# Optimization experiments

Measured on AMD Instinct MI355X. Metric: run time of the kernel, lower is better.

The kernel has to match this reference:

```python
import jax, jax.numpy as jnp
import numpy as np

N = 50000
E = 800000
CIN = 32
COUT = 64
DIM = 2
KS = 5                      # kernel size per pseudo-coordinate dim
K = KS ** DIM               # 25 kernel weight matrices
DEGREE = 1
S = (DEGREE + 1) ** DIM     # 4 nonzero B-spline basis products per edge


def _spline_basis(pseudo):
    # pseudo: [E, DIM] in [0, 1]; open linear (degree-1) B-splines per dim.
    v = pseudo * (KS - DEGREE)                              # [E, DIM]
    lo = jnp.floor(v)
    frac = v - lo                                           # [E, DIM]
    lo = jnp.clip(lo.astype(jnp.int32), 0, KS - 2)          # guard p == 1
    bits = (jnp.arange(S)[:, None] >> jnp.arange(DIM)[None, :]) & 1   # [S, DIM]
    # tensor-product basis values: [E, S]
    b = jnp.where(bits[None].astype(bool), frac[:, None, :], 1.0 - frac[:, None, :])
    basis = jnp.prod(b, axis=-1)
    offsets = (KS ** jnp.arange(DIM)).astype(jnp.int32)     # flat-index strides
    wi = jnp.sum((lo[:, None, :] + bits[None]) * offsets[None, None, :], axis=-1)  # [E, S]
    return basis, wi


def setup_inputs() -> dict:
    key = jax.random.key(0)
    k1, k2, k3, k4, k5, k6 = jax.random.split(key, 6)
    bound = 1.0 / np.sqrt(CIN * K)
    x = jax.random.normal(k1, (N, CIN), dtype=jnp.float32)
    edge_index = jax.random.randint(k2, (2, E), 0, N, dtype=jnp.int64)
    pseudo = jax.random.uniform(k3, (E, DIM), dtype=jnp.float32)
    weight = jax.random.uniform(k4, (K, CIN, COUT), minval=-bound, maxval=bound, dtype=jnp.float32)
    root = jax.random.uniform(k5, (CIN, COUT), minval=-bound, maxval=bound, dtype=jnp.float32)
    bias = jax.random.uniform(k6, (COUT,), minval=-bound, maxval=bound, dtype=jnp.float32)
    return {"x": x, "edge_index": edge_index, "pseudo": pseudo,
            "weight": weight, "root": root, "bias": bias}


def reference(x, edge_index, pseudo, weight, root, bias):
    n, cin = x.shape
    cout = weight.shape[-1]
    row = edge_index[0]   # destination nodes (scatter target)
    col = edge_index[1]   # source nodes (gather)
    basis, wi = _spline_basis(pseudo)                       # [E, S], [E, S]
    # Transform every node by every kernel weight matrix: [N, K, Cout]
    y = jnp.einsum('ni,kio->nko', x, weight)
    flat = y.reshape(n * K, cout)
    g = flat[col[:, None] * K + wi]                         # [E, S, Cout] gather
    msg = jnp.einsum('es,eso->eo', basis, g)                # [E, Cout]
    out = jax.ops.segment_sum(msg, row, num_segments=n)     # scatter-add to dst
    deg = jax.ops.segment_sum(jnp.ones((row.shape[0],), dtype=x.dtype), row, num_segments=n)
    out = out / jnp.maximum(deg, 1.0)[:, None]              # degree normalization
    out = out + x @ root + bias                             # root transform + bias
    return out
```

## Files before the change

kernel.cpp:

```cpp
#include <hip/hip_runtime.h>

#define N_NODES 50000
#define E_EDGES 800000
#define CIN     32
#define COUT    64
#define NB      16
#define BCAP    54016
#define NCB     196
#define RCAP    4864
#define KPAD    136
#define SCANB   1024
#define NSCANBLK ((N_NODES + SCANB - 1) / SCANB)
#define EPB     8
#define BBLK    ((E_EDGES + EPB * 256 - 1) / (EPB * 256))
#define XCHUNK  (N_NODES * CIN / 4)

typedef __attribute__((ext_vector_type(8))) short s8v;
typedef __attribute__((ext_vector_type(4))) float f4v;
typedef __attribute__((ext_vector_type(4))) unsigned short u4v;

static __device__ inline unsigned short f2bf(float f) {
    unsigned u = __builtin_bit_cast(unsigned, f);
    u += 0x7fff + ((u >> 16) & 1);
    return (unsigned short)(u >> 16);
}
static __device__ inline float bf2f(unsigned short h) {
    unsigned u = ((unsigned)h) << 16;
    return __builtin_bit_cast(float, u);
}
static __device__ inline unsigned f2bf2(float a, float b) {
    return (unsigned)f2bf(a) | ((unsigned)f2bf(b) << 16);
}


__global__ __launch_bounds__(256) void build_recs(
    const float* __restrict__ x, unsigned short* __restrict__ xbf,
    const int* __restrict__ ei, const float* __restrict__ pseudo,
    int* __restrict__ cursor, int* __restrict__ cursR,
    unsigned long long* __restrict__ recs, unsigned* __restrict__ rp)
{
    {
        const int cb = blockIdx.x * 1024;
#pragma unroll
        for (int k = 0; k < 4; ++k) {
            const int i = cb + k * 256 + threadIdx.x;
            if (i < XCHUNK) {
                f4v v = *(const f4v*)(x + (size_t)i * 4);
                union { unsigned u2[2]; u4v v4; } o;
                o.u2[0] = f2bf2(v[0], v[1]);
                o.u2[1] = f2bf2(v[2], v[3]);
                *(u4v*)(xbf + (size_t)i * 4) = o.v4;
            }
        }
    }

    __shared__ int lh[NB];
    __shared__ int lbase[NB];
    __shared__ int lh2[NCB];
    __shared__ int lbase2[NCB];
    if (threadIdx.x < NB) lh[threadIdx.x] = 0;
    if (threadIdx.x < NCB) lh2[threadIdx.x] = 0;
    __syncthreads();

    const int ebase0 = blockIdx.x * (EPB * 256);
    unsigned long long rcache[EPB];
    int pcache[EPB];
    int pcache2[EPB];

#pragma unroll
    for (int i = 0; i < EPB; ++i) {
        const int e = ebase0 + i * 256 + threadIdx.x;
        pcache[i] = -1; pcache2[i] = -1;
        if (e < E_EDGES) {
            const int row = min(max(ei[e], 0), N_NODES - 1);
            const int col = min(max(ei[E_EDGES + e], 0), N_NODES - 1);
            const float v0 = pseudo[2 * e] * 4.0f, v1 = pseudo[2 * e + 1] * 4.0f;
            const float fl0 = floorf(v0), fl1 = floorf(v1);
            const int lo0 = min(max((int)fl0, 0), 3);
            const int lo1 = min(max((int)fl1, 0), 3);
            const int f0q = min((int)((v0 - fl0) * 65536.0f), 65535);
            const int f1q = min((int)((v1 - fl1) * 65536.0f), 65535);
            const int b = lo0 + 4 * lo1;
            rcache[i] = (unsigned long long)row
                      | ((unsigned long long)col << 16)
                      | ((unsigned long long)f0q << 32)
                      | ((unsigned long long)f1q << 48);
            pcache[i]  = b | (atomicAdd(&lh[b], 1) << 8);
            const int cb = row >> 8;
            pcache2[i] = cb | (atomicAdd(&lh2[cb], 1) << 8);
        }
    }
    __syncthreads();

    if (threadIdx.x < NB)
        lbase[threadIdx.x] = atomicAdd(&cursor[threadIdx.x], lh[threadIdx.x]);
    if (threadIdx.x < NCB)
        lbase2[threadIdx.x] = atomicAdd(&cursR[threadIdx.x], lh2[threadIdx.x]);
    __syncthreads();

#pragma unroll
    for (int i = 0; i < EPB; ++i) {
        if (pcache[i] >= 0) {
            const int b = pcache[i] & 0xFF;
            const int idx = min(lbase[b] + (pcache[i] >> 8), BCAP - 1);
            const unsigned recslot = (unsigned)(b * BCAP + idx);
            recs[recslot] = rcache[i];
            const int cb = pcache2[i] & 0xFF;
            const int idx2 = min(lbase2[cb] + (pcache2[i] >> 8), RCAP - 1);
            const unsigned rowlow = (unsigned)(rcache[i] & 0xFF);
            rp[(size_t)cb * RCAP + idx2] = recslot | (rowlow << 20);
        }
    }
}

__global__ __launch_bounds__(256) void deg_hist(
    const unsigned* __restrict__ rp, const int* __restrict__ cursR,
    int* __restrict__ degi)
{
    __shared__ int h[256];
    h[threadIdx.x] = 0;
    __syncthreads();
    const int cb = blockIdx.x;
    const int cnt = min(cursR[cb], RCAP);
    const unsigned* bp = rp + (size_t)cb * RCAP;
    for (int i = threadIdx.x; i < cnt; i += 256)
        atomicAdd(&h[bp[i] >> 20], 1);
    __syncthreads();
    const int row = cb * 256 + threadIdx.x;
    if (row < N_NODES) degi[row] = h[threadIdx.x];
}

__global__ __launch_bounds__(1024) void scan_blocks(
    const int* __restrict__ degi, int* __restrict__ rowstart, int* __restrict__ bsum)
{
    __shared__ int wsum[16];
    __shared__ int woff[16];
    const int tid = threadIdx.x, lane = tid & 63, wid = tid >> 6;
    const int n = blockIdx.x * SCANB + tid;
    const int v = (n < N_NODES) ? degi[n] : 0;
    int val = v;
#pragma unroll
    for (int off = 1; off < 64; off <<= 1) {
        int t = __shfl_up(val, off);
        if (lane >= off) val += t;
    }
    if (lane == 63) wsum[wid] = val;
    __syncthreads();
    if (tid == 0) {
        int a = 0;
#pragma unroll
        for (int w = 0; w < 16; ++w) { woff[w] = a; a += wsum[w]; }
        bsum[blockIdx.x] = a;
    }
    __syncthreads();
    if (n < N_NODES) rowstart[n] = woff[wid] + (val - v);
}

__global__ __launch_bounds__(1024) void scan_finish(
    int* __restrict__ rowstart, const int* __restrict__ bsum)
{
    const int b = blockIdx.x;
    int off = 0;
    for (int i = 0; i < NSCANBLK; ++i)
        off += (i < b) ? bsum[i] : 0;
    const int n = b * SCANB + threadIdx.x;
    if (n < N_NODES) rowstart[n] += off;
    if (b == NSCANBLK - 1 && threadIdx.x == 0)
        rowstart[N_NODES] = off + bsum[NSCANBLK - 1];
}

__global__ __launch_bounds__(256) void rank_write(
    const unsigned* __restrict__ rp, const int* __restrict__ cursR,
    const int* __restrict__ rowstart, unsigned* __restrict__ eidx)
{
    __shared__ int cur[256];
    const int cb = blockIdx.x;
    const int row = cb * 256 + threadIdx.x;
    cur[threadIdx.x] = (row < N_NODES) ? rowstart[row] : 0;
    __syncthreads();
    const int cnt = min(cursR[cb], RCAP);
    const unsigned* bp = rp + (size_t)cb * RCAP;
    for (int i = threadIdx.x; i < cnt; i += 256) {
        const unsigned e = bp[i];
        const int pos = min(atomicAdd(&cur[e >> 20], 1), E_EDGES - 1);
        eidx[pos] = e & 0xFFFFF;
    }
}

__global__ __launch_bounds__(256, 2) void bucket_mfma_seq(
    const unsigned short* __restrict__ xbf, const float* __restrict__ weight,
    const unsigned long long* __restrict__ recs,
    const int* __restrict__ cursor, const int* __restrict__ degi,
    unsigned short* __restrict__ msg)
{
    __shared__ short XS[4][16 * KPAD];

    const int lane = threadIdx.x & 63;
    const int wid  = threadIdx.x >> 6;
    const int cell = blockIdx.x & (NB - 1);
    const int wGlob   = (blockIdx.x >> 4) * 4 + wid;
    const int wStride = (gridDim.x >> 4) * 4;
    const int eg = lane >> 2, part = lane & 3;

    const int lo0 = cell & 3, lo1 = cell >> 2;
    const int base = lo0 + 5 * lo1;
    const int offs[4] = {0, 1, 5, 6};
    const int q = lane >> 4;
    const int c = lane & 15;

    s8v bfr[4][4];
#pragma unroll
    for (int s = 0; s < 4; ++s) {
        const float* wp = weight + (size_t)(base + offs[s]) * (CIN * COUT);
#pragma unroll
        for (int nt = 0; nt < 4; ++nt) {
            union { unsigned short u[8]; s8v v; } tmp;
#pragma unroll
            for (int j = 0; j < 8; ++j)
                tmp.u[j] = f2bf(wp[(q * 8 + j) * COUT + nt * 16 + c]);
            bfr[s][nt] = tmp.v;
        }
    }

    const unsigned long long* brec = recs + (size_t)cell * BCAP;
    const int cnt    = min(cursor[cell], BCAP);
    const int ntiles = (cnt + 15) >> 4;

    int t = wGlob;
    unsigned long long rec_c = 0;
    int deg_c = 1;
    s8v x_c = {};
    if (t < ntiles) {
        rec_c = brec[min(t * 16 + eg, cnt - 1)];
        deg_c = degi[(int)(rec_c & 0xFFFF)];
        x_c = *(const s8v*)(xbf + (size_t)((rec_c >> 16) & 0xFFFF) * CIN + part * 8);
    }

    for (; t < ntiles; t += wStride) {
        const int tn = t + wStride;
        unsigned long long rec_n = 0;
        int deg_n = 1;
        if (tn < ntiles) {
            rec_n = brec[min(tn * 16 + eg, cnt - 1)];
            deg_n = degi[(int)(rec_n & 0xFFFF)];
        }

        const bool vcur = (t * 16 + eg) < cnt;
        const float f0 = (float)(int)((rec_c >> 32) & 0xFFFF) * (1.0f / 65536.0f);
        const float f1 = (float)(int)((rec_c >> 48) & 0xFFFF) * (1.0f / 65536.0f);
        const float invd = vcur ? (1.0f / (float)max(deg_c, 1)) : 0.0f;
        const float s0 = (1.0f - f0) * (1.0f - f1) * invd;
        const float s1 = f0 * (1.0f - f1) * invd;
        const float s2 = (1.0f - f0) * f1 * invd;
        const float s3 = f0 * f1 * invd;

        {
            union { unsigned short u[8]; s8v v; } xin; xin.v = x_c;
            float xv[8];
#pragma unroll
            for (int j = 0; j < 8; ++j) xv[j] = bf2f(xin.u[j]);
            short* dst = &XS[wid][eg * KPAD + part * 8];
            const float ss[4] = {s0, s1, s2, s3};
#pragma unroll
            for (int s = 0; s < 4; ++s) {
                union { unsigned u2[4]; s8v v; } tmp;
#pragma unroll
                for (int j = 0; j < 8; j += 2)
                    tmp.u2[j >> 1] = f2bf2(ss[s] * xv[j], ss[s] * xv[j + 1]);
                *(s8v*)(dst + s * 32) = tmp.v;
            }
        }
        __builtin_amdgcn_wave_barrier();

        s8v afr[4];
        {
            const short* ap = &XS[wid][c * KPAD + q * 8];
#pragma unroll
            for (int ks = 0; ks < 4; ++ks)
                afr[ks] = *(const s8v*)(ap + ks * 32);
        }
        __builtin_amdgcn_wave_barrier();

        s8v x_n = {};
        if (tn < ntiles)
            x_n = *(const s8v*)(xbf + (size_t)((rec_n >> 16) & 0xFFFF) * CIN + part * 8);

        f4v acc[4];
#pragma unroll
        for (int nt = 0; nt < 4; ++nt) {
            acc[nt] = (f4v){0.f, 0.f, 0.f, 0.f};
#pragma unroll
            for (int ks = 0; ks < 4; ++ks)
                acc[nt] = __builtin_amdgcn_mfma_f32_16x16x32_bf16(
                    afr[ks], bfr[ks][nt], acc[nt], 0, 0, 0);
        }

#pragma unroll
        for (int r = 0; r < 4; ++r) {
            const int m = q * 4 + r;
#pragma unroll
            for (int nt = 0; nt < 4; ++nt)
                XS[wid][m * 64 + nt * 16 + c] = (short)f2bf(acc[nt][r]);
        }
        __builtin_amdgcn_wave_barrier();
        {
            const short* sp = &XS[wid][eg * 64 + part * 16];
            s8v vlo = *(const s8v*)sp;
            s8v vhi = *(const s8v*)(sp + 8);
            unsigned short* dst = msg
                + ((size_t)cell * BCAP + (size_t)t * 16 + eg) * COUT + part * 16;
            *(s8v*)dst = vlo;
            *(s8v*)(dst + 8) = vhi;
        }
        __builtin_amdgcn_wave_barrier();

        rec_c = rec_n; deg_c = deg_n; x_c = x_n;
    }
}

__global__ __launch_bounds__(256) void gather_perm(
    const unsigned short* __restrict__ msg, const unsigned* __restrict__ eidx,
    const int* __restrict__ rowstart, const float* __restrict__ x,
    const float* __restrict__ root, const float* __restrict__ bias,
    float* __restrict__ out)
{
    const int wave   = (blockIdx.x * blockDim.x + threadIdx.x) >> 6;
    const int lane   = threadIdx.x & 63;
    const int nwaves = (gridDim.x * blockDim.x) >> 6;

    for (int n = wave; n < N_NODES; n += nwaves) {
        const int s  = rowstart[n];
        const int e2 = rowstart[n + 1];
        float acc = 0.f;
#pragma unroll 8
        for (int p = s; p < e2; ++p) {
            const unsigned slot = eidx[p];
            acc += bf2f(msg[(size_t)slot * COUT + lane]);
        }
        const float* xp = x + (size_t)n * CIN;
        float rt = bias[lane];
#pragma unroll
        for (int i = 0; i < CIN; ++i)
            rt += xp[i] * root[i * COUT + lane];
        out[(size_t)n * COUT + lane] = acc + rt;
    }
}


__global__ __launch_bounds__(256) void count_fb(
    const int* __restrict__ ei, const float* __restrict__ pseudo,
    int* __restrict__ hist, float* __restrict__ deg)
{
    __shared__ int lh[16];
    if (threadIdx.x < 16) lh[threadIdx.x] = 0;
    __syncthreads();
    const int e = blockIdx.x * 256 + threadIdx.x;
    if (e < E_EDGES) {
        int row = min(max(ei[e], 0), N_NODES - 1);
        const float v0 = pseudo[2 * e] * 4.0f, v1 = pseudo[2 * e + 1] * 4.0f;
        const int lo0 = min(max((int)floorf(v0), 0), 3);
        const int lo1 = min(max((int)floorf(v1), 0), 3);
        atomicAdd(&lh[lo0 + 4 * lo1], 1);
        atomicAdd(&deg[row], 1.0f);
    }
    __syncthreads();
    if (threadIdx.x < 16) atomicAdd(&hist[threadIdx.x], lh[threadIdx.x]);
}

__global__ void scan16_fb(const int* __restrict__ hist,
                          int* __restrict__ bstart, int* __restrict__ cursor)
{
    if (threadIdx.x == 0 && blockIdx.x == 0) {
        int acc = 0;
        for (int c = 0; c < 16; ++c) { bstart[c] = acc; cursor[c] = acc; acc += hist[c]; }
    }
}

__global__ __launch_bounds__(256) void scatter_fb(
    const float* __restrict__ pseudo, int* __restrict__ cursor, int* __restrict__ list)
{
    __shared__ int lh[16];
    __shared__ int lbase[16];
    if (threadIdx.x < 16) lh[threadIdx.x] = 0;
    __syncthreads();
    const int e = blockIdx.x * 256 + threadIdx.x;
    int cell = 0, myoff = 0;
    if (e < E_EDGES) {
        const float v0 = pseudo[2 * e] * 4.0f, v1 = pseudo[2 * e + 1] * 4.0f;
        const int lo0 = min(max((int)floorf(v0), 0), 3);
        const int lo1 = min(max((int)floorf(v1), 0), 3);
        cell = lo0 + 4 * lo1;
        myoff = atomicAdd(&lh[cell], 1);
    }
    __syncthreads();
    if (threadIdx.x < 16)
        lbase[threadIdx.x] = atomicAdd(&cursor[threadIdx.x], lh[threadIdx.x]);
    __syncthreads();
    if (e < E_EDGES)
        list[lbase[cell] + myoff] = e;
}

__global__ __launch_bounds__(256, 2) void bucket_mfma_fb(
    const float* __restrict__ x, const int* __restrict__ ei,
    const float* __restrict__ pseudo, const float* __restrict__ weight,
    const int* __restrict__ list, const int* __restrict__ bstart,
    const int* __restrict__ hist, float* __restrict__ out)
{
    __shared__ short XS[4][16 * KPAD];
    const int lane = threadIdx.x & 63;
    const int wid  = threadIdx.x >> 6;
    const int beta = blockIdx.x & 15;
    const int wGlob   = (blockIdx.x >> 4) * 4 + wid;
    const int wStride = (gridDim.x >> 4) * 4;
    const int lo0 = beta & 3, lo1 = beta >> 2;
    const int base = lo0 + 5 * lo1;
    const int offs[4] = {0, 1, 5, 6};
    const int q = lane >> 4, c = lane & 15;

    s8v bfr[4][4];
#pragma unroll
    for (int s = 0; s < 4; ++s) {
        const float* wp = weight + (size_t)(base + offs[s]) * (CIN * COUT);
#pragma unroll
        for (int nt = 0; nt < 4; ++nt) {
            union { unsigned short u[8]; s8v v; } tmp;
#pragma unroll
            for (int j = 0; j < 8; ++j)
                tmp.u[j] = f2bf(wp[(q * 8 + j) * COUT + nt * 16 + c]);
            bfr[s][nt] = tmp.v;
        }
    }
    const int start = bstart[beta], cnt = hist[beta];
    const int ntiles = (cnt + 15) >> 4;

    for (int t = wGlob; t < ntiles; t += wStride) {
        const int ebase = start + t * 16;
        int rowv = 0, colv = 0;
        float b0 = 0.f, b1 = 0.f, b2 = 0.f, b3 = 0.f;
        if (lane < 16 && (t * 16 + lane) < cnt) {
            const int e = list[ebase + lane];
            rowv = min(max(ei[e], 0), N_NODES - 1);
            colv = min(max(ei[E_EDGES + e], 0), N_NODES - 1);
            const float v0 = pseudo[2 * e] * 4.0f, v1 = pseudo[2 * e + 1] * 4.0f;
            const float f0 = v0 - floorf(v0), f1 = v1 - floorf(v1);
            b0 = (1.0f - f0) * (1.0f - f1);
            b1 = f0 * (1.0f - f1);
            b2 = (1.0f - f0) * f1;
            b3 = f0 * f1;
        }
        {
            const int eg = lane >> 2, part = lane & 3;
            const int  gc = __shfl(colv, eg);
            const float ss0 = __shfl(b0, eg), ss1 = __shfl(b1, eg);
            const float ss2 = __shfl(b2, eg), ss3 = __shfl(b3, eg);
            const float ss[4] = {ss0, ss1, ss2, ss3};
            const float* xp = x + (size_t)gc * CIN + part * 8;
            float xv[8];
            *(f4v*)&xv[0] = *(const f4v*)xp;
            *(f4v*)&xv[4] = *(const f4v*)(xp + 4);
            short* dst = &XS[wid][eg * KPAD + part * 8];
#pragma unroll
            for (int s = 0; s < 4; ++s) {
                union { unsigned short u[8]; s8v v; } tmp;
#pragma unroll
                for (int j = 0; j < 8; ++j)
                    tmp.u[j] = f2bf(ss[s] * xv[j]);
                *(s8v*)(dst + s * 32) = tmp.v;
            }
        }
        __builtin_amdgcn_wave_barrier();
        s8v afr[4];
        {
            const short* ap = &XS[wid][c * KPAD + q * 8];
#pragma unroll
            for (int ks = 0; ks < 4; ++ks)
                afr[ks] = *(const s8v*)(ap + ks * 32);
        }
        __builtin_amdgcn_wave_barrier();
        f4v acc[4];
#pragma unroll
        for (int nt = 0; nt < 4; ++nt) {
            acc[nt] = (f4v){0.f, 0.f, 0.f, 0.f};
#pragma unroll
            for (int ks = 0; ks < 4; ++ks)
                acc[nt] = __builtin_amdgcn_mfma_f32_16x16x32_bf16(
                    afr[ks], bfr[ks][nt], acc[nt], 0, 0, 0);
        }
#pragma unroll
        for (int r = 0; r < 4; ++r) {
            const int m = q * 4 + r;
            const int orow = __shfl(rowv, m);
#pragma unroll
            for (int nt = 0; nt < 4; ++nt)
                atomicAdd(&out[(size_t)orow * COUT + nt * 16 + c], acc[nt][r]);
        }
    }
}

__global__ __launch_bounds__(256) void final_fb(
    const float* __restrict__ x, const float* __restrict__ root,
    const float* __restrict__ bias, const float* __restrict__ deg,
    float* __restrict__ out)
{
    const int wave   = (blockIdx.x * blockDim.x + threadIdx.x) >> 6;
    const int lane   = threadIdx.x & 63;
    const int nwaves = (gridDim.x * blockDim.x) >> 6;
    for (int n = wave; n < N_NODES; n += nwaves) {
        const float* xp = x + (size_t)n * CIN;
        float acc = bias[lane];
#pragma unroll
        for (int i = 0; i < CIN; ++i)
            acc += xp[i] * root[i * COUT + lane];
        float dg = deg[n];
        dg = dg > 1.0f ? dg : 1.0f;
        const size_t idx = (size_t)n * COUT + lane;
        out[idx] = out[idx] / dg + acc;
    }
}

extern "C" void kernel_launch(void* const* d_in, const int* in_sizes, int n_in,
                              void* d_out, int out_size, void* d_ws, size_t ws_size,
                              hipStream_t stream) {
    const float* x      = (const float*)d_in[0];
    const int*   ei     = (const int*)d_in[1];
    const float* pseudo = (const float*)d_in[2];
    const float* weight = (const float*)d_in[3];
    const float* root   = (const float*)d_in[4];
    const float* bias   = (const float*)d_in[5];
    float* out = (float*)d_out;

    int* wsI = (int*)d_ws;
    int* cursor16 = wsI;
    int* cursR    = wsI + 32;
    int* degi     = wsI + 256;
    int* rowstart = wsI + 50256;
    int* bsum     = wsI + 100272;
    unsigned long long* recs = (unsigned long long*)((char*)d_ws + 401408);
    unsigned* rp   = (unsigned*)((char*)d_ws + 401408 + (size_t)NB * BCAP * 8);
    unsigned* eidx = (unsigned*)((char*)rp + (size_t)NCB * RCAP * 4);
    unsigned short* xbf = (unsigned short*)((char*)eidx + (size_t)E_EDGES * 4);
    unsigned short* msg = (unsigned short*)((char*)xbf + (size_t)N_NODES * CIN * 2);
    const size_t needed = 401408 + (size_t)NB * BCAP * 8 + (size_t)NCB * RCAP * 4
                        + (size_t)E_EDGES * 4 + (size_t)N_NODES * CIN * 2
                        + (size_t)NB * BCAP * COUT * 2;

    if (ws_size >= needed) {
        (void)hipMemsetAsync(d_ws, 0, 256 * 4, stream);
        build_recs <<<BBLK, 256, 0, stream>>>(x, xbf, ei, pseudo, cursor16, cursR, recs, rp);
        deg_hist   <<<NCB, 256, 0, stream>>>(rp, cursR, degi);
        scan_blocks<<<NSCANBLK, 1024, 0, stream>>>(degi, rowstart, bsum);
        scan_finish<<<NSCANBLK, 1024, 0, stream>>>(rowstart, bsum);
        rank_write <<<NCB, 256, 0, stream>>>(rp, cursR, rowstart, eidx);
        bucket_mfma_seq<<<16 * 128, 256, 0, stream>>>(
            xbf, weight, recs, cursor16, degi, msg);
        gather_perm<<<4096, 256, 0, stream>>>(msg, eidx, rowstart, x, root, bias, out);
    } else {
        char* w = (char*)d_ws;
        float* degF   = (float*)w;
        int*   histF  = (int*)(w + 200064);
        int*   bstF   = (int*)(w + 200128);
        int*   curF   = (int*)(w + 200192);
        int*   listF  = (int*)(w + 200256);
        const int eblocks = (E_EDGES + 255) / 256;

        (void)hipMemsetAsync(out, 0, sizeof(float) * (size_t)N_NODES * COUT, stream);
        (void)hipMemsetAsync(degF, 0, sizeof(float) * (size_t)N_NODES, stream);
        (void)hipMemsetAsync(histF, 0, 192, stream);

        count_fb      <<<eblocks, 256, 0, stream>>>(ei, pseudo, histF, degF);
        scan16_fb     <<<1, 64, 0, stream>>>(histF, bstF, curF);
        scatter_fb    <<<eblocks, 256, 0, stream>>>(pseudo, curF, listF);
        bucket_mfma_fb<<<16 * 64, 256, 0, stream>>>(x, ei, pseudo, weight, listF,
                                                    bstF, histF, out);
        final_fb      <<<1024, 256, 0, stream>>>(x, root, bias, degF, out);
    }
}
```

Baseline: 196.6 us.

## Scatter messages directly to destination-sorted slots and gather them contiguously

rank_write now records each edge's destination-sorted position (dpos) instead of an inverse index list. The MFMA kernel writes each message row straight into that sorted slot, so the gather kernel reads contiguous message rows per node with 16-byte loads. The gather also splits edges across 8 lane groups, keeps root and bias in registers, and reduces across groups with shuffles. The cost is scattered 128-byte writes in the MFMA kernel instead of sequential ones, in exchange for dropping the eidx indirection and the 2-byte-per-lane random reads in the gather.

Measured after the change: 179.3 us. -8.8%, faster.

```diff
diff --git a/kernel.cpp b/kernel.cpp
--- a/kernel.cpp
+++ b/kernel.cpp
@@ -171,7 +171,7 @@
 
 __global__ __launch_bounds__(256) void rank_write(
     const unsigned* __restrict__ rp, const int* __restrict__ cursR,
-    const int* __restrict__ rowstart, unsigned* __restrict__ eidx)
+    const int* __restrict__ rowstart, int* __restrict__ dpos)
 {
     __shared__ int cur[256];
     const int cb = blockIdx.x;
@@ -183,7 +183,7 @@
     for (int i = threadIdx.x; i < cnt; i += 256) {
         const unsigned e = bp[i];
         const int pos = min(atomicAdd(&cur[e >> 20], 1), E_EDGES - 1);
-        eidx[pos] = e & 0xFFFFF;
+        dpos[e & 0xFFFFF] = pos;
     }
 }
 
@@ -191,7 +191,7 @@
     const unsigned short* __restrict__ xbf, const float* __restrict__ weight,
     const unsigned long long* __restrict__ recs,
     const int* __restrict__ cursor, const int* __restrict__ degi,
-    unsigned short* __restrict__ msg)
+    const int* __restrict__ dpos, unsigned short* __restrict__ msg)
 {
     __shared__ short XS[4][16 * KPAD];
 
@@ -223,16 +223,20 @@
     }
 
     const unsigned long long* brec = recs + (size_t)cell * BCAP;
+    const int* bdp = dpos + (size_t)cell * BCAP;
     const int cnt    = min(cursor[cell], BCAP);
     const int ntiles = (cnt + 15) >> 4;
 
     int t = wGlob;
     unsigned long long rec_c = 0;
     int deg_c = 1;
+    int dp_c  = 0;
     s8v x_c = {};
     if (t < ntiles) {
-        rec_c = brec[min(t * 16 + eg, cnt - 1)];
+        const int ri = min(t * 16 + eg, cnt - 1);
+        rec_c = brec[ri];
         deg_c = degi[(int)(rec_c & 0xFFFF)];
+        dp_c  = bdp[ri];
         x_c = *(const s8v*)(xbf + (size_t)((rec_c >> 16) & 0xFFFF) * CIN + part * 8);
     }
 
@@ -240,9 +244,12 @@
         const int tn = t + wStride;
         unsigned long long rec_n = 0;
         int deg_n = 1;
+        int dp_n  = 0;
         if (tn < ntiles) {
-            rec_n = brec[min(tn * 16 + eg, cnt - 1)];
+            const int ri = min(tn * 16 + eg, cnt - 1);
+            rec_n = brec[ri];
             deg_n = degi[(int)(rec_n & 0xFFFF)];
+            dp_n  = bdp[ri];
         }
 
         const bool vcur = (t * 16 + eg) < cnt;
@@ -303,23 +310,22 @@
                 XS[wid][m * 64 + nt * 16 + c] = (short)f2bf(acc[nt][r]);
         }
         __builtin_amdgcn_wave_barrier();
-        {
-            const short* sp = &XS[wid][eg * 64 + part * 16];
+        if (vcur) {
+            const short* sp = &XS[wid][eg * 64 + part * 8];
             s8v vlo = *(const s8v*)sp;
-            s8v vhi = *(const s8v*)(sp + 8);
-            unsigned short* dst = msg
-                + ((size_t)cell * BCAP + (size_t)t * 16 + eg) * COUT + part * 16;
+            s8v vhi = *(const s8v*)(sp + 32);
+            unsigned short* dst = msg + (size_t)dp_c * COUT + part * 8;
             *(s8v*)dst = vlo;
-            *(s8v*)(dst + 8) = vhi;
+            *(s8v*)(dst + 32) = vhi;
         }
         __builtin_amdgcn_wave_barrier();
 
-        rec_c = rec_n; deg_c = deg_n; x_c = x_n;
-    }
-}
-
-__global__ __launch_bounds__(256) void gather_perm(
-    const unsigned short* __restrict__ msg, const unsigned* __restrict__ eidx,
+        rec_c = rec_n; deg_c = deg_n; dp_c = dp_n; x_c = x_n;
+    }
+}
+
+__global__ __launch_bounds__(256) void gather_seq(
+    const unsigned short* __restrict__ msg,
     const int* __restrict__ rowstart, const float* __restrict__ x,
     const float* __restrict__ root, const float* __restrict__ bias,
     float* __restrict__ out)
@@ -327,22 +333,59 @@
     const int wave   = (blockIdx.x * blockDim.x + threadIdx.x) >> 6;
     const int lane   = threadIdx.x & 63;
     const int nwaves = (gridDim.x * blockDim.x) >> 6;
+    const int g = lane >> 3;
+    const int c = lane & 7;
+
+    float rfr[4][8];
+#pragma unroll
+    for (int i = 0; i < 4; ++i) {
+        const int ii = g * 4 + i;
+        *(f4v*)&rfr[i][0] = *(const f4v*)(root + (size_t)ii * COUT + c * 8);
+        *(f4v*)&rfr[i][4] = *(const f4v*)(root + (size_t)ii * COUT + c * 8 + 4);
+    }
+    float bs[8];
+    *(f4v*)&bs[0] = *(const f4v*)(bias + c * 8);
+    *(f4v*)&bs[4] = *(const f4v*)(bias + c * 8 + 4);
 
     for (int n = wave; n < N_NODES; n += nwaves) {
         const int s  = rowstart[n];
         const int e2 = rowstart[n + 1];
-        float acc = 0.f;
-#pragma unroll 8
-        for (int p = s; p < e2; ++p) {
-            const unsigned slot = eidx[p];
-            acc += bf2f(msg[(size_t)slot * COUT + lane]);
-        }
-        const float* xp = x + (size_t)n * CIN;
-        float rt = bias[lane];
-#pragma unroll
-        for (int i = 0; i < CIN; ++i)
-            rt += xp[i] * root[i * COUT + lane];
-        out[(size_t)n * COUT + lane] = acc + rt;
+        float acc[8] = {0.f, 0.f, 0.f, 0.f, 0.f, 0.f, 0.f, 0.f};
+
+        for (int p = s + g; p < e2; p += 8) {
+            union { s8v v; unsigned short u[8]; } mv;
+            mv.v = *(const s8v*)(msg + (size_t)p * COUT + c * 8);
+#pragma unroll
+            for (int j = 0; j < 8; ++j)
+                acc[j] += bf2f(mv.u[j]);
+        }
+
+        const f4v xv4 = *(const f4v*)(x + (size_t)n * CIN + g * 4);
+#pragma unroll
+        for (int i = 0; i < 4; ++i) {
+            const float xv = xv4[i];
+#pragma unroll
+            for (int j = 0; j < 8; ++j)
+                acc[j] += xv * rfr[i][j];
+        }
+
+#pragma unroll
+        for (int off = 8; off < 64; off <<= 1) {
+#pragma unroll
+            for (int j = 0; j < 8; ++j)
+                acc[j] += __shfl_xor(acc[j], off);
+        }
+
+        if (g == 0) {
+            f4v o0, o1;
+#pragma unroll
+            for (int j = 0; j < 4; ++j) o0[j] = acc[j] + bs[j];
+#pragma unroll
+            for (int j = 0; j < 4; ++j) o1[j] = acc[4 + j] + bs[4 + j];
+            float* op = out + (size_t)n * COUT + c * 8;
+            *(f4v*)op = o0;
+            *(f4v*)(op + 4) = o1;
+        }
     }
 }
 
@@ -536,13 +579,13 @@
     int* rowstart = wsI + 50256;
     int* bsum     = wsI + 100272;
     unsigned long long* recs = (unsigned long long*)((char*)d_ws + 401408);
-    unsigned* rp   = (unsigned*)((char*)d_ws + 401408 + (size_t)NB * BCAP * 8);
-    unsigned* eidx = (unsigned*)((char*)rp + (size_t)NCB * RCAP * 4);
-    unsigned short* xbf = (unsigned short*)((char*)eidx + (size_t)E_EDGES * 4);
+    unsigned* rp   = (unsigned*)((char*)recs + (size_t)NB * BCAP * 8);
+    int* dpos      = (int*)((char*)rp + (size_t)NCB * RCAP * 4);
+    unsigned short* xbf = (unsigned short*)((char*)dpos + (size_t)NB * BCAP * 4);
     unsigned short* msg = (unsigned short*)((char*)xbf + (size_t)N_NODES * CIN * 2);
     const size_t needed = 401408 + (size_t)NB * BCAP * 8 + (size_t)NCB * RCAP * 4
-                        + (size_t)E_EDGES * 4 + (size_t)N_NODES * CIN * 2
-                        + (size_t)NB * BCAP * COUT * 2;
+                        + (size_t)NB * BCAP * 4 + (size_t)N_NODES * CIN * 2
+                        + (size_t)E_EDGES * COUT * 2;
 
     if (ws_size >= needed) {
         (void)hipMemsetAsync(d_ws, 0, 256 * 4, stream);
@@ -550,10 +593,10 @@
         deg_hist   <<<NCB, 256, 0, stream>>>(rp, cursR, degi);
         scan_blocks<<<NSCANBLK, 1024, 0, stream>>>(degi, rowstart, bsum);
         scan_finish<<<NSCANBLK, 1024, 0, stream>>>(rowstart, bsum);
-        rank_write <<<NCB, 256, 0, stream>>>(rp, cursR, rowstart, eidx);
+        rank_write <<<NCB, 256, 0, stream>>>(rp, cursR, rowstart, dpos);
         bucket_mfma_seq<<<16 * 128, 256, 0, stream>>>(
-            xbf, weight, recs, cursor16, degi, msg);
-        gather_perm<<<4096, 256, 0, stream>>>(msg, eidx, rowstart, x, root, bias, out);
+            xbf, weight, recs, cursor16, degi, dpos, msg);
+        gather_seq<<<4096, 256, 0, stream>>>(msg, rowstart, x, root, bias, out);
     } else {
         char* w = (char*)d_ws;
         float* degF   = (float*)w;
```
